# Optimization experiments

Measured on AMD Instinct MI355X. Metric: run time of the kernel, lower is better.

Reference implementation:

```python
import jax, jax.numpy as jnp
import numpy as np

B, Hd, Wd, C, NH, WS = 8, 128, 128, 192, 6, 8
HDIM = int(C * 2.0)   # FFN hidden = 384
RED = C // 8          # AIM channel-gate reduction = 24


def setup_inputs() -> dict:
    key = jax.random.key(0)
    ks = jax.random.split(key, 12)
    s = 0.02
    return {
        "x": jax.random.normal(ks[0], (B, Hd * Wd, C), jnp.float32),
        "H": Hd,
        "W": Wd,
        "n1_w": jnp.ones((C,), jnp.float32),
        "n1_b": jnp.zeros((C,), jnp.float32),
        "qkv_w": jax.random.normal(ks[1], (C, 3 * C), jnp.float32) * s,
        "proj_w": jax.random.normal(ks[2], (C, C), jnp.float32) * s,
        "proj_b": jnp.zeros((C,), jnp.float32),
        "attn_bias": jax.random.normal(ks[3], (NH, WS * WS, WS * WS), jnp.float32) * s,
        "conv_w": jax.random.normal(ks[4], (C, 1, 3, 3), jnp.float32) * s,
        "cg_w1": jax.random.normal(ks[5], (RED, C), jnp.float32) * s,
        "cg_w2": jax.random.normal(ks[6], (C, RED), jnp.float32) * s,
        "n2_w": jnp.ones((C,), jnp.float32),
        "n2_b": jnp.zeros((C,), jnp.float32),
        "fc1_w": jax.random.normal(ks[7], (C, HDIM), jnp.float32) * s,
        "smix_w": jax.random.normal(ks[8], (HDIM, 1, 3, 3), jnp.float32) * s,
        "fc2_w": jax.random.normal(ks[9], (HDIM, C), jnp.float32) * s,
    }


def _ln(x, w, b):
    m = x.mean(-1, keepdims=True)
    v = ((x - m) ** 2).mean(-1, keepdims=True)
    return (x - m) * jax.lax.rsqrt(v + 1e-5) * w + b


def _dwconv(x, w, H, W):
    # x: [B, L, Cx] -> depthwise 3x3 'same' conv -> [B, L, Cx]
    Bx, L, Cx = x.shape
    xi = x.transpose(0, 2, 1).reshape(Bx, Cx, H, W)
    y = jax.lax.conv_general_dilated(
        xi, w, (1, 1), 'SAME', feature_group_count=Cx,
        dimension_numbers=('NCHW', 'OIHW', 'NCHW'))
    return y.reshape(Bx, Cx, L).transpose(0, 2, 1)


def _window_attn(x, H, W, qkv_w, proj_w, proj_b, bias):
    Bx, L, Cx = x.shape
    nHw, nWw = H // WS, W // WS  # H, W are multiples of WS here (no padding needed)
    hd = Cx // NH
    # [B, L, C] -> [B*nH*nW, ws*ws, C]
    xw = (x.reshape(Bx, nHw, WS, nWw, WS, Cx)
           .transpose(0, 1, 3, 2, 4, 5)
           .reshape(Bx * nHw * nWw, WS * WS, Cx))
    qkv = (xw @ qkv_w).reshape(-1, WS * WS, 3, NH, hd).transpose(2, 0, 3, 1, 4)
    q, k, v = qkv[0], qkv[1], qkv[2]          # [Bw, nh, N, hd]
    logits = (q * hd ** -0.5) @ k.transpose(0, 1, 3, 2) + bias[None]
    attn = jax.nn.softmax(logits, axis=-1)
    out = (attn @ v).transpose(0, 2, 1, 3).reshape(-1, WS * WS, Cx)
    out = out @ proj_w + proj_b
    # windows -> [B, L, C]
    return (out.reshape(Bx, nHw, nWw, WS, WS, Cx)
               .transpose(0, 1, 3, 2, 4, 5)
               .reshape(Bx, L, Cx))


def reference(x, H, W, n1_w, n1_b, qkv_w, proj_w, proj_b, attn_bias,
              conv_w, cg_w1, cg_w2, n2_w, n2_b, fc1_w, smix_w, fc2_w):
    n1 = _ln(x, n1_w, n1_b)
    attn_feat = _window_attn(n1, H, W, qkv_w, proj_w, proj_b, attn_bias)
    conv_feat = jax.nn.gelu(_dwconv(n1, conv_w, H, W), approximate=False)
    # AIM: channel_modulates_spatial (btype == 'spatial')
    pooled = conv_feat.mean(axis=1)                                   # [B, C]
    cm = jax.nn.sigmoid(jax.nn.gelu(pooled @ cg_w1.T, approximate=False) @ cg_w2.T)
    x = x + attn_feat * cm[:, None, :] + conv_feat                    # residual (DropPath=id)
    # FFN with depthwise spatial mixing
    n2 = _ln(x, n2_w, n2_b)
    h = jax.nn.gelu(n2 @ fc1_w, approximate=False)                    # [B, L, HDIM]
    h = _dwconv(h, smix_w, H, W)
    return x + h @ fc2_w
```

## Files before the change

### kernel.cpp

```cpp
#include <hip/hip_runtime.h>
#include <hip/hip_bf16.h>
#include <math.h>

#define BATCH 8
#define CCH 192
#define LTOK 16384
#define BL 131072LL
#define NWIN 2048
#define NHEADS 6

typedef __hip_bfloat16 bf16;
typedef __bf16 bfr;
typedef bfr bf16x8 __attribute__((ext_vector_type(8)));
typedef float f32x4 __attribute__((ext_vector_type(4)));
typedef unsigned short u16x8 __attribute__((ext_vector_type(8)));
typedef unsigned short u16x4 __attribute__((ext_vector_type(4)));
typedef unsigned int u32x2 __attribute__((ext_vector_type(2)));

#define FX     0
#define FN1W   1
#define FN1B   2
#define FQKVW  3
#define FPROJW 4
#define FPROJB 5
#define FBIAS  6
#define FCONVW 7
#define FCG1   8
#define FCG2   9
#define FN2W   10
#define FN2B   11
#define FFC1   12
#define FSMIX  13
#define FFC2   14

struct InPtrs { const void* p[15]; int n[15]; };

__device__ __forceinline__ float ldin(const void* p, long long i, int f32) {
    return f32 ? ((const float*)p)[i]
               : __bfloat162float(((const bf16*)p)[i]);
}

__device__ __forceinline__ float bfcvt(unsigned short u) {
    return __uint_as_float((unsigned)u << 16);
}

__device__ __forceinline__ f32x4 ld4f(const void* p, long long i, int f32) {
    if (f32) return *(const f32x4*)((const float*)p + i);
    u16x4 v = *(const u16x4*)((const bf16*)p + i);
    f32x4 r;
    r[0] = bfcvt(v[0]); r[1] = bfcvt(v[1]); r[2] = bfcvt(v[2]); r[3] = bfcvt(v[3]);
    return r;
}
__device__ __forceinline__ f32x4 ld4b(const bf16* p, long long i) {
    u16x4 v = *(const u16x4*)(p + i);
    f32x4 r;
    r[0] = bfcvt(v[0]); r[1] = bfcvt(v[1]); r[2] = bfcvt(v[2]); r[3] = bfcvt(v[3]);
    return r;
}
__device__ __forceinline__ void st4b(bf16* p, long long i, f32x4 v) {
    union { bf16 h; unsigned short u; } cv;
    u16x4 o;
    cv.h = __float2bfloat16(v[0]); o[0] = cv.u;
    cv.h = __float2bfloat16(v[1]); o[1] = cv.u;
    cv.h = __float2bfloat16(v[2]); o[2] = cv.u;
    cv.h = __float2bfloat16(v[3]); o[3] = cv.u;
    *(u16x4*)(p + i) = o;
}

__device__ __forceinline__ unsigned pk2bf(float a, float b) {
    union { bf16 h; unsigned short u; } ca, cb;
    ca.h = __float2bfloat16(a);
    cb.h = __float2bfloat16(b);
    return (unsigned)ca.u | ((unsigned)cb.u << 16);
}

__device__ __forceinline__ float gelu_f(float v) {
    return 0.5f * v * (1.0f + erff(v * 0.70710678118654752f));
}

__device__ int local_probe(const void* p_, int n) {
    __shared__ int sh0, sh1, sh2;
    if (threadIdx.x == 0) { sh0 = 0; sh1 = 0; sh2 = 0; }
    __syncthreads();
    const bf16* p = (const bf16*)p_;
    int m = n < 2048 ? n : 2048;
    bool insane = false, evennz = false, oddnz = false;
    for (int i = threadIdx.x; i < m; i += 256) {
        float v = __bfloat162float(p[i]);
        if (!(fabsf(v) <= 1e9f)) insane = true;
        if (v != 0.0f) { if (i & 1) oddnz = true; else evennz = true; }
    }
    if (insane) sh0 = 1;
    if (evennz) sh1 = 1;
    if (oddnz)  sh2 = 1;
    __syncthreads();
    return (sh0 || (!sh1 && sh2)) ? 1 : 0;
}

__global__ __launch_bounds__(256)
void prep_k(InPtrs ip, int* __restrict__ flags,
            bf16* __restrict__ qkv_wT, bf16* __restrict__ proj_wT,
            bf16* __restrict__ fc1_wT, bf16* __restrict__ fc2_wT,
            float* __restrict__ convwT, float* __restrict__ smixwT,
            float* __restrict__ pooled) {
    int blk = blockIdx.x;
    if (blk < 15) {
        int f = local_probe(ip.p[blk], ip.n[blk]);
        if (threadIdx.x == 0) flags[blk] = f;
        return;
    }
    blk -= 15;
    if (blk < 432) {
        int f = local_probe(ip.p[FQKVW], ip.n[FQKVW]);
        int idx = blk * 256 + threadIdx.x;
        int k = idx / 576, n = idx - k * 576;
        qkv_wT[(long long)n * 192 + k] = __float2bfloat16(ldin(ip.p[FQKVW], idx, f));
        return;
    }
    blk -= 432;
    if (blk < 144) {
        int f = local_probe(ip.p[FPROJW], ip.n[FPROJW]);
        int idx = blk * 256 + threadIdx.x;
        int k = idx / 192, n = idx - k * 192;
        proj_wT[(long long)n * 192 + k] = __float2bfloat16(ldin(ip.p[FPROJW], idx, f));
        return;
    }
    blk -= 144;
    if (blk < 288) {
        int f = local_probe(ip.p[FFC1], ip.n[FFC1]);
        int idx = blk * 256 + threadIdx.x;
        int k = idx / 384, n = idx - k * 384;
        fc1_wT[(long long)n * 192 + k] = __float2bfloat16(ldin(ip.p[FFC1], idx, f));
        return;
    }
    blk -= 288;
    if (blk < 288) {
        int f = local_probe(ip.p[FFC2], ip.n[FFC2]);
        int idx = blk * 256 + threadIdx.x;
        int k = idx / 192, n = idx - k * 192;
        fc2_wT[(long long)n * 384 + k] = __float2bfloat16(ldin(ip.p[FFC2], idx, f));
        return;
    }
    blk -= 288;
    if (blk < 7) {
        int f = local_probe(ip.p[FCONVW], ip.n[FCONVW]);
        int idx = blk * 256 + threadIdx.x;
        if (idx < 192 * 9) {
            int c = idx / 9, t = idx - c * 9;
            convwT[t * 192 + c] = ldin(ip.p[FCONVW], idx, f);
        }
        return;
    }
    blk -= 7;
    if (blk < 14) {
        int f = local_probe(ip.p[FSMIX], ip.n[FSMIX]);
        int idx = blk * 256 + threadIdx.x;
        if (idx < 384 * 9) {
            int c = idx / 9, t = idx - c * 9;
            smixwT[t * 384 + c] = ldin(ip.p[FSMIX], idx, f);
        }
        return;
    }
    blk -= 14;
    {
        int idx = blk * 256 + threadIdx.x;
        if (idx < BATCH * CCH) pooled[idx] = 0.f;
    }
}

__global__ __launch_bounds__(256)
void ln_kernel(const void* __restrict__ x, const void* __restrict__ w,
               const void* __restrict__ b, bf16* __restrict__ out,
               const int* flags) {
    int fx = flags[FX], fw = flags[FN1W], fb = flags[FN1B];
    int wv = threadIdx.x >> 6, lane = threadIdx.x & 63;
    int gw = lane >> 4, l16 = lane & 15;
    long long t = (long long)blockIdx.x * 16 + wv * 4 + gw;
    long long base = t * CCH;
    f32x4 v[3];
#pragma unroll
    for (int k = 0; k < 3; ++k)
        v[k] = ld4f(x, base + l16 * 4 + 64 * k, fx);
    float s = 0.f;
#pragma unroll
    for (int k = 0; k < 3; ++k) s += v[k][0] + v[k][1] + v[k][2] + v[k][3];
    s += __shfl_xor(s, 1); s += __shfl_xor(s, 2);
    s += __shfl_xor(s, 4); s += __shfl_xor(s, 8);
    float mean = s * (1.0f / 192.0f);
    float vs = 0.f;
#pragma unroll
    for (int k = 0; k < 3; ++k)
#pragma unroll
        for (int j = 0; j < 4; ++j) {
            float d = v[k][j] - mean;
            vs += d * d;
        }
    vs += __shfl_xor(vs, 1); vs += __shfl_xor(vs, 2);
    vs += __shfl_xor(vs, 4); vs += __shfl_xor(vs, 8);
    float rstd = rsqrtf(vs * (1.0f / 192.0f) + 1e-5f);
#pragma unroll
    for (int k = 0; k < 3; ++k) {
        int c0 = l16 * 4 + 64 * k;
        f32x4 wv4 = ld4f(w, c0, fw);
        f32x4 bv4 = ld4f(b, c0, fb);
        f32x4 o;
#pragma unroll
        for (int j = 0; j < 4; ++j)
            o[j] = (v[k][j] - mean) * rstd * wv4[j] + bv4[j];
        st4b(out, base + c0, o);
    }
}

template<int EPI, int KK, int NN, typename CT>
__global__ __launch_bounds__(256)
void gemm2_k(const bf16* __restrict__ A_, const bf16* __restrict__ BT_,
             CT* __restrict__ Cmat, const void* __restrict__ bias,
             const float* __restrict__ res, const int* __restrict__ flags) {
    constexpr int KT = KK / 192;
    constexpr int NC = NN / 64;
    constexpr int NITER = NC * KT;
    constexpr int GSTR = KK * 2;
    constexpr bool WINM = (EPI == 0);
    __shared__ __align__(16) char Ts[64 * 384];

    const int fb = (EPI == 1) ? flags[FPROJB] : 0;
    const int tid = threadIdx.x;
    const int lane = tid & 63, wv = tid >> 6;
    const int r16 = lane & 15, q = lane >> 4;
    const long long m0 = (long long)blockIdx.x * 64;
    const int swz = (r16 & 7) << 4;

    const int wdx = blockIdx.x;
    const int wb = wdx >> 8, wrem = wdx & 255, wy = wrem >> 4, wx = wrem & 15;
    const long long tokbase = (long long)wb * LTOK + (wy * 8) * 128 + wx * 8;

    f32x4 pre[6];
    auto loadB = [&](int itn) {
        int nc2 = itn / KT, kt2 = itn - nc2 * KT;
#pragma unroll
        for (int p = 0; p < 6; ++p) {
            int off = p * 4096 + tid * 16;
            int row = off / 384, col = off - row * 384;
            pre[p] = *(const f32x4*)((const char*)BT_ +
                     (long long)(nc2 * 64 + row) * GSTR + kt2 * 384 + col);
        }
    };
    auto writeT = [&]() {
#pragma unroll
        for (int p = 0; p < 6; ++p) {
            int off = p * 4096 + tid * 16;
            int row = off / 384, col = off - row * 384;
            *(f32x4*)(Ts + row * 384 + (col ^ ((row & 7) << 4))) = pre[p];
        }
    };

    loadB(0);

    bf16x8 afrag[KK / 32];
    const char* Arow = Ts + (wv * 16 + r16) * 384;
    const char* asrc = (const char*)A_;
#pragma unroll
    for (int kt = 0; kt < KT; ++kt) {
#pragma unroll
        for (int p = 0; p < 6; ++p) {
            int off = p * 4096 + tid * 16;
            int row = off / 384, col = off - row * 384;
            long long grow = WINM ? (tokbase + (row >> 3) * 128 + (row & 7))
                                  : (m0 + row);
            *(f32x4*)(Ts + row * 384 + (col ^ ((row & 7) << 4))) =
                *(const f32x4*)(asrc + grow * GSTR + kt * 384 + col);
        }
        __syncthreads();
#pragma unroll
        for (int ks = 0; ks < 6; ++ks)
            afrag[kt * 6 + ks] = *(const bf16x8*)(Arow + ((ks * 64 + q * 16) ^ swz));
        __syncthreads();
    }
    writeT();
    __syncthreads();

    f32x4 acc0, acc1, acc2, acc3;
    float resv[16];

    for (int it = 0; it < NITER; ++it) {
        const int nc = it / KT, kt = it - nc * KT;
        if (kt == 0) {
            acc0 = f32x4{0.f, 0.f, 0.f, 0.f};
            acc1 = acc0; acc2 = acc0; acc3 = acc0;
            if (EPI == 3) {
#pragma unroll
                for (int j = 0; j < 4; ++j)
#pragma unroll
                    for (int r = 0; r < 4; ++r)
                        resv[j * 4 + r] =
                            res[(m0 + wv * 16 + q * 4 + r) * NN + nc * 64 + j * 16 + r16];
            }
        }
        const bool nxt = (it + 1 < NITER);
        if (nxt) loadB(it + 1);
#pragma unroll
        for (int ks = 0; ks < 6; ++ks) {
            bf16x8 a = afrag[kt * 6 + ks];
            const char* bb = Ts + r16 * 384 + ((ks * 64 + q * 16) ^ swz);
            bf16x8 b0 = *(const bf16x8*)(bb);
            bf16x8 b1 = *(const bf16x8*)(bb + 16 * 384);
            bf16x8 b2 = *(const bf16x8*)(bb + 32 * 384);
            bf16x8 b3 = *(const bf16x8*)(bb + 48 * 384);
            acc0 = __builtin_amdgcn_mfma_f32_16x16x32_bf16(a, b0, acc0, 0, 0, 0);
            acc1 = __builtin_amdgcn_mfma_f32_16x16x32_bf16(a, b1, acc1, 0, 0, 0);
            acc2 = __builtin_amdgcn_mfma_f32_16x16x32_bf16(a, b2, acc2, 0, 0, 0);
            acc3 = __builtin_amdgcn_mfma_f32_16x16x32_bf16(a, b3, acc3, 0, 0, 0);
        }
        __syncthreads();
        if (nxt) writeT();
        if (kt == KT - 1) {
            f32x4 accs[4] = {acc0, acc1, acc2, acc3};
#pragma unroll
            for (int j = 0; j < 4; ++j) {
                int col = nc * 64 + j * 16 + r16;
#pragma unroll
                for (int r = 0; r < 4; ++r) {
                    float v = accs[j][r];
                    if (EPI == 1) v += ldin(bias, col, fb);
                    if (EPI == 2) v = gelu_f(v);
                    if (EPI == 3) v += resv[j * 4 + r];
                    if (WINM) {
                        int tin = wv * 16 + q * 4 + r;
                        int sel = col / 192, rem2 = col - sel * 192;
                        int hh = rem2 >> 5, d = rem2 & 31;
                        Cmat[((((long long)sel * NWIN + wdx) * 6 + hh) * 64 + tin) * 32 + d] = (CT)v;
                    } else {
                        long long row = m0 + wv * 16 + q * 4 + r;
                        Cmat[row * NN + col] = (CT)v;
                    }
                }
            }
        }
        if (nxt) __syncthreads();
    }
}

__global__ __launch_bounds__(768)
void attn_proj_k(const bf16* __restrict__ qkvw, const void* __restrict__ bias,
                 const bf16* __restrict__ pwT, const void* __restrict__ proj_b,
                 bf16* __restrict__ attnf, const int* __restrict__ flags) {
    __shared__ __align__(16) char SM[24576];

    const int fbias = flags[FBIAS];
    const int wid = threadIdx.x >> 6, lane = threadIdx.x & 63;
    const int h = wid >> 1, half = wid & 1;
    const int w = blockIdx.x;
    const int l15 = lane & 15, quad = lane >> 4;
    bfr* vtp = (bfr*)(SM + h * 4096);

    const bfr* qb = (const bfr*)qkvw + ((long long)w * 6 + h) * 2048;
    const bfr* kb = qb + (long long)NWIN * 6 * 2048;
    const bfr* vb = kb + (long long)NWIN * 6 * 2048;

    if (half == 0) {
        const bfr* vp = vb + lane * 32;
        bf16x8 v0 = *(const bf16x8*)(vp);
        bf16x8 v1 = *(const bf16x8*)(vp + 8);
        bf16x8 v2 = *(const bf16x8*)(vp + 16);
        bf16x8 v3 = *(const bf16x8*)(vp + 24);
#pragma unroll
        for (int j = 0; j < 8; ++j) {
            int sc = lane ^ (j << 3);
            vtp[j * 64 + sc]        = v0[j];
            vtp[(j + 8) * 64 + sc]  = v1[j];
            vtp[(j + 16) * 64 + sc] = v2[j];
            vtp[(j + 24) * 64 + sc] = v3[j];
        }
    }

    bf16x8 bk[4], aq[2];
#pragma unroll
    for (int ti = 0; ti < 4; ++ti)
        bk[ti] = *(const bf16x8*)(kb + (ti * 16 + l15) * 32 + quad * 8);
#pragma unroll
    for (int tj2 = 0; tj2 < 2; ++tj2)
        aq[tj2] = *(const bf16x8*)(qb + ((half * 2 + tj2) * 16 + l15) * 32 + quad * 8);

    const float scale = 0.17677669529663689f;
    const long long bias0 = (long long)h * 4096;
    unsigned Wreg[2][4][2];
#pragma unroll
    for (int tj2 = 0; tj2 < 2; ++tj2) {
        const int tj = half * 2 + tj2;
        f32x4 T[4];
        __builtin_amdgcn_s_setprio(1);
#pragma unroll
        for (int ti = 0; ti < 4; ++ti) {
            f32x4 z = {0.f, 0.f, 0.f, 0.f};
            T[ti] = __builtin_amdgcn_mfma_f32_16x16x32_bf16(bk[ti], aq[tj2], z, 0, 0, 0);
        }
        __builtin_amdgcn_s_setprio(0);
        const long long brow = bias0 + (tj * 16 + l15) * 64 + quad * 4;
        float mloc = -3.0e38f;
#pragma unroll
        for (int ti = 0; ti < 4; ++ti) {
            f32x4 bv4 = ld4f(bias, brow + ti * 16, fbias);
#pragma unroll
            for (int r = 0; r < 4; ++r) {
                float v = T[ti][r] * scale + bv4[r];
                T[ti][r] = v;
                mloc = fmaxf(mloc, v);
            }
        }
        mloc = fmaxf(mloc, __shfl_xor(mloc, 16));
        mloc = fmaxf(mloc, __shfl_xor(mloc, 32));
        float l = 0.f;
#pragma unroll
        for (int ti = 0; ti < 4; ++ti)
#pragma unroll
            for (int r = 0; r < 4; ++r) {
                float e = __expf(T[ti][r] - mloc);
                T[ti][r] = e;
                l += e;
            }
        l += __shfl_xor(l, 16);
        l += __shfl_xor(l, 32);
        float linv = 1.0f / l;
#pragma unroll
        for (int ti = 0; ti < 4; ++ti) {
            Wreg[tj2][ti][0] = pk2bf(T[ti][0] * linv, T[ti][1] * linv);
            Wreg[tj2][ti][1] = pk2bf(T[ti][2] * linv, T[ti][3] * linv);
        }
    }

    __syncthreads();

    const int vsw = (l15 & 7) << 3;
    bf16x8 bv[2][2];
#pragma unroll
    for (int kc = 0; kc < 2; ++kc) {
        bv[kc][0] = *(const bf16x8*)&vtp[l15 * 64 + ((kc * 32 + quad * 8) ^ vsw)];
        bv[kc][1] = *(const bf16x8*)&vtp[(16 + l15) * 64 + ((kc * 32 + quad * 8) ^ vsw)];
    }
    const int hi = quad >> 1, qlow = quad & 1;
    f32x4 O[2][2];
#pragma unroll
    for (int tj2 = 0; tj2 < 2; ++tj2) {
        O[tj2][0] = f32x4{0.f, 0.f, 0.f, 0.f};
        O[tj2][1] = O[tj2][0];
    }
#pragma unroll
    for (int tj2 = 0; tj2 < 2; ++tj2)
#pragma unroll
        for (int kc = 0; kc < 2; ++kc) {
            union { unsigned u[4]; bf16x8 v; } ap;
#pragma unroll
            for (int j2 = 0; j2 < 4; ++j2) {
                int srcl = (2 * qlow + (j2 >> 1)) * 16 + l15;
                unsigned va = (unsigned)__shfl((int)Wreg[tj2][2 * kc][j2 & 1], srcl);
                unsigned vb2 = (unsigned)__shfl((int)Wreg[tj2][2 * kc + 1][j2 & 1], srcl);
                ap.u[j2] = hi ? vb2 : va;
            }
            __builtin_amdgcn_s_setprio(1);
            O[tj2][0] = __builtin_amdgcn_mfma_f32_16x16x32_bf16(ap.v, bv[kc][0], O[tj2][0], 0, 0, 0);
            O[tj2][1] = __builtin_amdgcn_mfma_f32_16x16x32_bf16(ap.v, bv[kc][1], O[tj2][1], 0, 0, 0);
            __builtin_amdgcn_s_setprio(0);
        }

    const int fpb = flags[FPROJB];
    const int pcol = wid * 16 + l15;
    float pbv = ldin(proj_b, pcol, fpb);
    bf16x8 pw[6];
#pragma unroll
    for (int ks = 0; ks < 6; ++ks)
        pw[ks] = *(const bf16x8*)((const bfr*)pwT + (long long)pcol * 192 + ks * 32 + quad * 8);

    __syncthreads();

#pragma unroll
    for (int tj2 = 0; tj2 < 2; ++tj2)
#pragma unroll
        for (int n2 = 0; n2 < 2; ++n2)
#pragma unroll
            for (int r = 0; r < 4; ++r) {
                int row = (half * 2 + tj2) * 16 + quad * 4 + r;
                int cb = (h * 64 + n2 * 32 + l15 * 2) ^ ((row & 7) << 4);
                *(bf16*)(SM + row * 384 + cb) = __float2bfloat16(O[tj2][n2][r]);
            }

    __syncthreads();

    const int csw = (l15 & 7) << 4;
    f32x4 pacc[4];
#pragma unroll
    for (int mt = 0; mt < 4; ++mt)
        pacc[mt] = f32x4{0.f, 0.f, 0.f, 0.f};
#pragma unroll
    for (int ks = 0; ks < 6; ++ks) {
#pragma unroll
        for (int mt = 0; mt < 4; ++mt) {
            bf16x8 af = *(const bf16x8*)(SM + (mt * 16 + l15) * 384 +
                                         ((ks * 64 + quad * 16) ^ csw));
            pacc[mt] = __builtin_amdgcn_mfma_f32_16x16x32_bf16(af, pw[ks], pacc[mt], 0, 0, 0);
        }
    }

#pragma unroll
    for (int mt = 0; mt < 4; ++mt)
#pragma unroll
        for (int r = 0; r < 4; ++r) {
            long long row = (long long)w * 64 + mt * 16 + quad * 4 + r;
            attnf[row * CCH + pcol] = __float2bfloat16(pacc[mt][r] + pbv);
        }
}

template<bool GELU, int CX, bool POOL>
__global__ __launch_bounds__(256)
void dwconv_s4_k(const bf16* __restrict__ in, const float* __restrict__ wt,
                 bf16* __restrict__ out, float* __restrict__ pooled) {
    constexpr int CG = CX / 8;
    __shared__ float psum[POOL ? 192 : 1];
    if (POOL) {
        if (threadIdx.x < 192) psum[threadIdx.x] = 0.f;
        __syncthreads();
    }
    int cpx = gridDim.x >> 3;
    int lb = (blockIdx.x & 7) * cpx + (blockIdx.x >> 3);
    long long idx = (long long)lb * 256 + threadIdx.x;
    int cg = (int)(idx % CG);
    long long s = idx / CG;
    int xs = (int)(s & 31);
    long long by = s >> 5;
    int y = (int)(by & 127);
    int x0 = xs * 4;
    int c0 = cg * 8;
    const long long rowpix = by * 128;

    float acc[4][8] = {};
#pragma unroll
    for (int dy = -1; dy <= 1; ++dy) {
        int yy = y + dy;
        if (yy < 0 || yy > 127) continue;
        const bf16* rp = in + ((rowpix + dy * 128) + x0) * CX + c0;
        float fcol[6][8];
#pragma unroll
        for (int ci = 0; ci < 6; ++ci) {
            int xx = x0 + ci - 1;
            if (xx < 0 || xx > 127) {
#pragma unroll
                for (int j = 0; j < 8; ++j) fcol[ci][j] = 0.f;
            } else {
                u16x8 v = *(const u16x8*)(rp + (ci - 1) * CX);
#pragma unroll
                for (int j = 0; j < 8; ++j) fcol[ci][j] = bfcvt(v[j]);
            }
        }
        const float* wb = wt + (dy + 1) * 3 * CX + c0;
#pragma unroll
        for (int dx = 0; dx < 3; ++dx) {
            f32x4 w0 = *(const f32x4*)(wb + dx * CX);
            f32x4 w1 = *(const f32x4*)(wb + dx * CX + 4);
#pragma unroll
            for (int px = 0; px < 4; ++px) {
#pragma unroll
                for (int j = 0; j < 4; ++j) {
                    acc[px][j]     += fcol[px + dx][j]     * w0[j];
                    acc[px][j + 4] += fcol[px + dx][j + 4] * w1[j];
                }
            }
        }
    }
    float sums[8] = {0.f, 0.f, 0.f, 0.f, 0.f, 0.f, 0.f, 0.f};
#pragma unroll
    for (int px = 0; px < 4; ++px) {
        __attribute__((aligned(16))) unsigned short ob[8];
#pragma unroll
        for (int j = 0; j < 8; ++j) {
            float vv = acc[px][j];
            if (GELU) vv = gelu_f(vv);
            if (POOL) sums[j] += vv;
            union { bf16 h; unsigned short u; } cv;
            cv.h = __float2bfloat16(vv);
            ob[j] = cv.u;
        }
        *(u16x8*)(out + (rowpix + x0 + px) * CX + c0) = *(const u16x8*)ob;
    }
    if (POOL) {
#pragma unroll
        for (int j = 0; j < 8; ++j)
            atomicAdd(&psum[c0 + j], sums[j]);
        __syncthreads();
        if (threadIdx.x < 192) {
            int b = (int)(by >> 7);
            atomicAdd(&pooled[b * CCH + threadIdx.x], psum[threadIdx.x]);
        }
    }
}

__global__ void cm_k(const float* __restrict__ pooled, const void* __restrict__ w1,
                     const void* __restrict__ w2, float* __restrict__ cm,
                     const int* flags) {
    __shared__ float ps[192], g[24];
    int f1 = flags[FCG1], f2 = flags[FCG2];
    int b = blockIdx.x, c = threadIdx.x;
    ps[c] = pooled[b * CCH + c] * (1.0f / 16384.0f);
    __syncthreads();
    if (c < 24) {
        float t = 0.f;
        for (int k = 0; k < 192; ++k) t += ps[k] * ldin(w1, c * 192 + k, f1);
        g[c] = gelu_f(t);
    }
    __syncthreads();
    float s = 0.f;
#pragma unroll
    for (int r = 0; r < 24; ++r) s += g[r] * ldin(w2, c * 24 + r, f2);
    cm[b * CCH + c] = 1.0f / (1.0f + expf(-s));
}

__global__ __launch_bounds__(256)
void x2ln2_k(const void* __restrict__ x, const bf16* __restrict__ attnf,
             const bf16* __restrict__ conv, const float* __restrict__ cm,
             const void* __restrict__ w, const void* __restrict__ bb,
             float* __restrict__ x2, bf16* __restrict__ n2, const int* flags) {
    int fx = flags[FX], fw = flags[FN2W], fb = flags[FN2B];
    int wv = threadIdx.x >> 6, lane = threadIdx.x & 63;
    int gw = lane >> 4, l16 = lane & 15;
    long long t = (long long)blockIdx.x * 16 + wv * 4 + gw;
    int b = (int)(t >> 14);
    int l = (int)(t & 16383);
    int y = l >> 7, xx = l & 127;
    long long wrow = ((long long)b * 256 + (y >> 3) * 16 + (xx >> 3)) * 64 + (y & 7) * 8 + (xx & 7);

    f32x4 sv[3];
#pragma unroll
    for (int k = 0; k < 3; ++k) {
        int c0 = l16 * 4 + 64 * k;
        f32x4 xv  = ld4f(x, t * CCH + c0, fx);
        f32x4 af  = ld4b(attnf, wrow * CCH + c0);
        f32x4 cf  = ld4b(conv, t * CCH + c0);
        f32x4 cmv = *(const f32x4*)(cm + b * CCH + c0);
        f32x4 o;
#pragma unroll
        for (int j = 0; j < 4; ++j)
            o[j] = xv[j] + af[j] * cmv[j] + cf[j];
        *(f32x4*)(x2 + t * CCH + c0) = o;
        sv[k] = o;
    }
    float s = 0.f;
#pragma unroll
    for (int k = 0; k < 3; ++k) s += sv[k][0] + sv[k][1] + sv[k][2] + sv[k][3];
    s += __shfl_xor(s, 1); s += __shfl_xor(s, 2);
    s += __shfl_xor(s, 4); s += __shfl_xor(s, 8);
    float mean = s * (1.0f / 192.0f);
    float vs = 0.f;
#pragma unroll
    for (int k = 0; k < 3; ++k)
#pragma unroll
        for (int j = 0; j < 4; ++j) {
            float d = sv[k][j] - mean;
            vs += d * d;
        }
    vs += __shfl_xor(vs, 1); vs += __shfl_xor(vs, 2);
    vs += __shfl_xor(vs, 4); vs += __shfl_xor(vs, 8);
    float rstd = rsqrtf(vs * (1.0f / 192.0f) + 1e-5f);
#pragma unroll
    for (int k = 0; k < 3; ++k) {
        int c0 = l16 * 4 + 64 * k;
        f32x4 wv4 = ld4f(w, c0, fw);
        f32x4 bv4 = ld4f(bb, c0, fb);
        f32x4 o;
#pragma unroll
        for (int j = 0; j < 4; ++j)
            o[j] = (sv[k][j] - mean) * rstd * wv4[j] + bv4[j];
        st4b(n2, t * CCH + c0, o);
    }
}

extern "C" void kernel_launch(void* const* d_in, const int* in_sizes, int n_in,
                              void* d_out, int out_size, void* d_ws, size_t ws_size,
                              hipStream_t stream) {
    (void)n_in; (void)out_size; (void)ws_size;
    float* out = (float*)d_out;

    char* wsp = (char*)d_ws;
    size_t off = 0;
    auto alloc = [&](size_t bytes) -> char* {
        char* p = wsp + off;
        off += (bytes + 255) & ~(size_t)255;
        return p;
    };
    int*  flags   = (int*)alloc(15 * 4);
    bf16* qkv_wT  = (bf16*)alloc(576 * 192 * 2);
    bf16* proj_wT = (bf16*)alloc(192 * 192 * 2);
    bf16* fc1_wT  = (bf16*)alloc(384 * 192 * 2);
    bf16* fc2_wT  = (bf16*)alloc(192 * 384 * 2);
    float* convwT = (float*)alloc(9 * CCH * 4);
    float* smixwT = (float*)alloc(9 * 384 * 4);
    float* pooled = (float*)alloc(BATCH * CCH * 4);
    float* cm     = (float*)alloc(BATCH * CCH * 4);
    char* Rbig    = alloc(BL * 576 * 2);
    char* Rpair   = alloc(BL * 384 * 2);

    bf16* qkvb  = (bf16*)Rbig;
    bf16* convf = (bf16*)Rbig;
    bf16* hbuf  = (bf16*)Rbig;
    bf16* n1    = (bf16*)Rpair;
    bf16* attnf = (bf16*)(Rpair + (size_t)BL * 192 * 2);
    bf16* n2    = n1;
    bf16* h2    = (bf16*)Rpair;
    float* x2   = out;

    const int imap[15] = {0, 3, 4, 5, 6, 7, 8, 9, 10, 11, 12, 13, 14, 15, 16};
    InPtrs ip;
    for (int i = 0; i < 15; ++i) { ip.p[i] = d_in[imap[i]]; ip.n[i] = in_sizes[imap[i]]; }
    const void* x        = d_in[0];
    const void* proj_b   = d_in[7];
    const void* attnbias = d_in[8];
    const void* cg_w1    = d_in[10];
    const void* cg_w2    = d_in[11];

    prep_k<<<1194, 256, 0, stream>>>(ip, flags, qkv_wT, proj_wT, fc1_wT, fc2_wT,
                                     convwT, smixwT, pooled);

    ln_kernel<<<BL / 16, 256, 0, stream>>>(x, d_in[3], d_in[4], n1, flags);
    gemm2_k<0, 192, 576, bf16><<<BL / 64, 256, 0, stream>>>(n1, qkv_wT, qkvb, nullptr, nullptr, flags);
    attn_proj_k<<<NWIN, 768, 0, stream>>>(qkvb, attnbias, proj_wT, proj_b, attnf, flags);
    dwconv_s4_k<true, 192, true><<<(int)(BL / 4 * 24 / 256), 256, 0, stream>>>(n1, convwT, convf, pooled);
    cm_k<<<BATCH, 192, 0, stream>>>(pooled, cg_w1, cg_w2, cm, flags);
    x2ln2_k<<<BL / 16, 256, 0, stream>>>(x, attnf, convf, cm, d_in[12], d_in[13], x2, n2, flags);
    gemm2_k<2, 192, 384, bf16><<<BL / 64, 256, 0, stream>>>(n2, fc1_wT, hbuf, nullptr, nullptr, flags);
    dwconv_s4_k<false, 384, false><<<(int)(BL / 4 * 48 / 256), 256, 0, stream>>>(hbuf, smixwT, h2, nullptr);
    gemm2_k<3, 384, 192, float><<<BL / 64, 256, 0, stream>>>(h2, fc2_wT, out, nullptr, x2, flags);
}
```

Baseline: 595.5 us.

## Split window attention blocks into half-window blocks with XCD-aware ordering

Each attention block now handles one half of a window's query rows (6 waves of 64 threads, one per head) rather than the whole window with 12 waves, which doubles the grid. Block indices are remapped so consecutive work items are spread across the 8 XCDs. Each block now loads the full V tile itself, removing a barrier, and each wave computes 32 projection columns for its 32 rows. The intent is better occupancy and scheduling from smaller blocks, at the cost of loading V and the projection weights twice per window.

```diff
diff --git a/kernel.cpp b/kernel.cpp
--- a/kernel.cpp
+++ b/kernel.cpp
@@ -340,7 +340,7 @@
     }
 }
 
-__global__ __launch_bounds__(768)
+__global__ __launch_bounds__(384)
 void attn_proj_k(const bf16* __restrict__ qkvw, const void* __restrict__ bias,
                  const bf16* __restrict__ pwT, const void* __restrict__ proj_b,
                  bf16* __restrict__ attnf, const int* __restrict__ flags) {
@@ -348,8 +348,9 @@
 
     const int fbias = flags[FBIAS];
     const int wid = threadIdx.x >> 6, lane = threadIdx.x & 63;
-    const int h = wid >> 1, half = wid & 1;
-    const int w = blockIdx.x;
+    const int h = wid;
+    const int work = (blockIdx.x & 7) * 512 + (blockIdx.x >> 3);
+    const int w = work >> 1, half = work & 1;
     const int l15 = lane & 15, quad = lane >> 4;
     bfr* vtp = (bfr*)(SM + h * 4096);
 
@@ -357,7 +358,7 @@
     const bfr* kb = qb + (long long)NWIN * 6 * 2048;
     const bfr* vb = kb + (long long)NWIN * 6 * 2048;
 
-    if (half == 0) {
+    {
         const bfr* vp = vb + lane * 32;
         bf16x8 v0 = *(const bf16x8*)(vp);
         bf16x8 v1 = *(const bf16x8*)(vp + 8);
@@ -428,7 +429,6 @@
         }
     }
 
-    __syncthreads();
 
     const int vsw = (l15 & 7) << 3;
     bf16x8 bv[2][2];
@@ -463,12 +463,16 @@
         }
 
     const int fpb = flags[FPROJB];
-    const int pcol = wid * 16 + l15;
-    float pbv = ldin(proj_b, pcol, fpb);
-    bf16x8 pw[6];
-#pragma unroll
-    for (int ks = 0; ks < 6; ++ks)
-        pw[ks] = *(const bf16x8*)((const bfr*)pwT + (long long)pcol * 192 + ks * 32 + quad * 8);
+    float pbv[2];
+    bf16x8 pw[2][6];
+#pragma unroll
+    for (int cg = 0; cg < 2; ++cg) {
+        int pcol = wid * 32 + cg * 16 + l15;
+        pbv[cg] = ldin(proj_b, pcol, fpb);
+#pragma unroll
+        for (int ks = 0; ks < 6; ++ks)
+            pw[cg][ks] = *(const bf16x8*)((const bfr*)pwT + (long long)pcol * 192 + ks * 32 + quad * 8);
+    }
 
     __syncthreads();
 
@@ -478,7 +482,7 @@
         for (int n2 = 0; n2 < 2; ++n2)
 #pragma unroll
             for (int r = 0; r < 4; ++r) {
-                int row = (half * 2 + tj2) * 16 + quad * 4 + r;
+                int row = tj2 * 16 + quad * 4 + r;
                 int cb = (h * 64 + n2 * 32 + l15 * 2) ^ ((row & 7) << 4);
                 *(bf16*)(SM + row * 384 + cb) = __float2bfloat16(O[tj2][n2][r]);
             }
@@ -486,27 +490,34 @@
     __syncthreads();
 
     const int csw = (l15 & 7) << 4;
-    f32x4 pacc[4];
-#pragma unroll
-    for (int mt = 0; mt < 4; ++mt)
-        pacc[mt] = f32x4{0.f, 0.f, 0.f, 0.f};
+    f32x4 pacc[2][2];
+#pragma unroll
+    for (int cg = 0; cg < 2; ++cg) {
+        pacc[cg][0] = f32x4{0.f, 0.f, 0.f, 0.f};
+        pacc[cg][1] = pacc[cg][0];
+    }
 #pragma unroll
     for (int ks = 0; ks < 6; ++ks) {
 #pragma unroll
-        for (int mt = 0; mt < 4; ++mt) {
+        for (int mt = 0; mt < 2; ++mt) {
             bf16x8 af = *(const bf16x8*)(SM + (mt * 16 + l15) * 384 +
                                          ((ks * 64 + quad * 16) ^ csw));
-            pacc[mt] = __builtin_amdgcn_mfma_f32_16x16x32_bf16(af, pw[ks], pacc[mt], 0, 0, 0);
-        }
-    }
-
-#pragma unroll
-    for (int mt = 0; mt < 4; ++mt)
-#pragma unroll
-        for (int r = 0; r < 4; ++r) {
-            long long row = (long long)w * 64 + mt * 16 + quad * 4 + r;
-            attnf[row * CCH + pcol] = __float2bfloat16(pacc[mt][r] + pbv);
-        }
+            pacc[0][mt] = __builtin_amdgcn_mfma_f32_16x16x32_bf16(af, pw[0][ks], pacc[0][mt], 0, 0, 0);
+            pacc[1][mt] = __builtin_amdgcn_mfma_f32_16x16x32_bf16(af, pw[1][ks], pacc[1][mt], 0, 0, 0);
+        }
+    }
+
+#pragma unroll
+    for (int cg = 0; cg < 2; ++cg) {
+        int pcol = wid * 32 + cg * 16 + l15;
+#pragma unroll
+        for (int mt = 0; mt < 2; ++mt)
+#pragma unroll
+            for (int r = 0; r < 4; ++r) {
+                long long row = (long long)w * 64 + half * 32 + mt * 16 + quad * 4 + r;
+                attnf[row * CCH + pcol] = __float2bfloat16(pacc[cg][mt][r] + pbv[cg]);
+            }
+    }
 }
 
 template<bool GELU, int CX, bool POOL>
@@ -719,7 +730,7 @@
 
     ln_kernel<<<BL / 16, 256, 0, stream>>>(x, d_in[3], d_in[4], n1, flags);
     gemm2_k<0, 192, 576, bf16><<<BL / 64, 256, 0, stream>>>(n1, qkv_wT, qkvb, nullptr, nullptr, flags);
-    attn_proj_k<<<NWIN, 768, 0, stream>>>(qkvb, attnbias, proj_wT, proj_b, attnf, flags);
+    attn_proj_k<<<NWIN * 2, 384, 0, stream>>>(qkvb, attnbias, proj_wT, proj_b, attnf, flags);
     dwconv_s4_k<true, 192, true><<<(int)(BL / 4 * 24 / 256), 256, 0, stream>>>(n1, convwT, convf, pooled);
     cm_k<<<BATCH, 192, 0, stream>>>(pooled, cg_w1, cg_w2, cm, flags);
     x2ln2_k<<<BL / 16, 256, 0, stream>>>(x, attnf, convf, cm, d_in[12], d_in[13], x2, n2, flags);
```

New measurement: 598.0 us. About the same (+0.4%).
